# Kernel optimization log

Hardware: AMD Instinct MI355X
Metric: run time of the kernel (lower is better)

## Reference

```python
import jax, jax.numpy as jnp
import numpy as np

LN_EPS = 1e-3  # keras LayerNormalization default epsilon


def setup_inputs() -> dict:
    key = jax.random.key(0)
    ks = jax.random.split(key, 6)
    B, S, D, H, K = 4, 4096, 1024, 16, 64
    scale = 1.0 / np.sqrt(D)
    return {
        "x": jax.random.normal(ks[0], (B, S, D), jnp.float32),
        "Wq": jax.random.normal(ks[1], (D, H, K), jnp.float32) * scale,
        "bq": jnp.zeros((H, K), jnp.float32),
        "Wk": jax.random.normal(ks[2], (D, H, K), jnp.float32) * scale,
        "bk": jnp.zeros((H, K), jnp.float32),
        "Wv": jax.random.normal(ks[3], (D, H, K), jnp.float32) * scale,
        "bv": jnp.zeros((H, K), jnp.float32),
        "Wo": jax.random.normal(ks[4], (H, K, D), jnp.float32) * scale,
        "bo": jnp.zeros((D,), jnp.float32),
        "gamma": jnp.ones((D,), jnp.float32),
        "beta": jnp.zeros((D,), jnp.float32),
        "num_window": 8,
    }


def reference(x, Wq, bq, Wk, bk, Wv, bv, Wo, bo, gamma, beta, num_window):
    B, S, D = x.shape
    H, K = Wq.shape[1], Wq.shape[2]
    Sw = S // num_window
    # Block-diagonal (windowed) attention: reshape seq into windows instead of a Python loop.
    xw = x.reshape(B, num_window, Sw, D)  # [B, W, Sw, D]
    q = jnp.einsum('bwsd,dhk->bwshk', xw, Wq) + bq
    k = jnp.einsum('bwsd,dhk->bwshk', xw, Wk) + bk
    v = jnp.einsum('bwsd,dhk->bwshk', xw, Wv) + bv
    scores = jnp.einsum('bwqhk,bwshk->bwhqs', q, k) / jnp.sqrt(jnp.asarray(K, x.dtype))
    attn = jax.nn.softmax(scores, axis=-1)  # [B, W, H, Sw, Sw]
    ctx = jnp.einsum('bwhqs,bwshk->bwqhk', attn, v)
    attn_out = (jnp.einsum('bwqhk,hkd->bwqd', ctx, Wo) + bo).reshape(B, S, D)
    # residual + layernorm (keras eps=1e-3)
    y = x + attn_out
    mu = jnp.mean(y, axis=-1, keepdims=True)
    var = jnp.mean(jnp.square(y - mu), axis=-1, keepdims=True)
    return (y - mu) * jax.lax.rsqrt(var + LN_EPS) * gamma + beta
```

## Files before the change

### kernel.cpp

```cpp
#include <hip/hip_runtime.h>

typedef __bf16 bf16_t;
typedef __bf16 bf16x4 __attribute__((ext_vector_type(4)));
typedef __bf16 bf16x8 __attribute__((ext_vector_type(8)));
typedef float f32x4 __attribute__((ext_vector_type(4)));

#define MFMA16(a, b, c) __builtin_amdgcn_mfma_f32_16x16x32_bf16((a), (b), (c), 0, 0, 0)

__device__ __forceinline__ void gl_lds16(const bf16_t* g, bf16_t* l) {
  __builtin_amdgcn_global_load_lds(
      (const __attribute__((address_space(1))) void*)g,
      (__attribute__((address_space(3))) void*)l, 16, 0, 0);
}

__global__ __launch_bounds__(256) void cast_x_kernel(const float* __restrict__ x,
                                                     bf16_t* __restrict__ xb) {
  size_t i = (size_t)blockIdx.x * 256 + threadIdx.x;
  float4 v = ((const float4*)x)[i];
  bf16x4 o = {(bf16_t)v.x, (bf16_t)v.y, (bf16_t)v.z, (bf16_t)v.w};
  ((bf16x4*)xb)[i] = o;
}

__global__ __launch_bounds__(256) void transpose_w_kernel(
    const float* __restrict__ Wq, const float* __restrict__ Wk,
    const float* __restrict__ Wv, const float* __restrict__ Wo,
    bf16_t* __restrict__ Wt, bf16_t* __restrict__ WoT) {
  __shared__ bf16_t T[64 * 68];
  const int z = blockIdx.z;
  const float* src = (z == 0) ? Wq : (z == 1) ? Wk : (z == 2) ? Wv : Wo;
  bf16_t* dst = (z < 3) ? (Wt + (size_t)z * 1024 * 1024) : WoT;
  const int tr = blockIdx.y * 64;
  const int tc = blockIdx.x * 64;
  const int tid = threadIdx.x;
#pragma unroll
  for (int it = 0; it < 4; ++it) {
    int t = tid + it * 256;
    int row = t >> 4, c4 = t & 15;
    float4 v = *(const float4*)&src[(size_t)(tr + row) * 1024 + tc + c4 * 4];
    bf16x4 o = {(bf16_t)v.x, (bf16_t)v.y, (bf16_t)v.z, (bf16_t)v.w};
    *(bf16x4*)&T[row * 68 + c4 * 4] = o;
  }
  __syncthreads();
#pragma unroll
  for (int it = 0; it < 2; ++it) {
    int t = tid + it * 256;
    int n = t >> 3, d8 = t & 7;
    bf16x8 o;
#pragma unroll
    for (int j = 0; j < 8; ++j) o[j] = T[(d8 * 8 + j) * 68 + n];
    *(bf16x8*)&dst[(size_t)(tc + n) * 1024 + tr + d8 * 8] = o;
  }
}


__device__ __forceinline__ void stage_half(const bf16_t* __restrict__ g,
                                           bf16_t* l, const int tid) {
#pragma unroll
  for (int j = 0; j < 2; ++j) {
    int idx = j * 512 + tid;
    int row = idx >> 3;
    int c = (idx & 7) ^ (row & 7);
    gl_lds16(g + (size_t)row * 1024 + c * 8, l + idx * 8);
  }
}

__device__ __forceinline__ void gemm256_main(const bf16_t* __restrict__ Ab,
                                             const bf16_t* __restrict__ Bb,
                                             bf16_t* lds, f32x4 (&acc)[8][4],
                                             const int tid) {
  const int l15 = tid & 15, quad = (tid >> 4) & 3;
  const int wv = tid >> 6, wm = wv >> 2, wn = wv & 3;
  const int sx = l15 & 7;
  const int brow0 = (wn & 1) * 64;

  stage_half(Bb, lds + 2 * 8192, tid);
  stage_half(Ab, lds + 0 * 8192, tid);
  stage_half(Bb + 128 * 1024, lds + 3 * 8192, tid);
  stage_half(Ab + 128 * 1024, lds + 1 * 8192, tid);
  stage_half(Bb + 64, lds + 6 * 8192, tid);
  stage_half(Ab + 64, lds + 4 * 8192, tid);
  asm volatile("s_waitcnt vmcnt(4)" ::: "memory");
  __builtin_amdgcn_s_barrier();

  for (int t = 0; t < 16; ++t) {
    bf16_t* const buf = lds + (t & 1) * 32768;
    bf16_t* const nbuf = lds + ((t & 1) ^ 1) * 32768;
    const bf16_t* const Ar = buf + wm * 8192;
    const bf16_t* const Br = buf + (2 + (wn >> 1)) * 8192;

    bf16x8 af[4][2], bfr[4][2];

#pragma unroll
    for (int mf = 0; mf < 4; ++mf)
#pragma unroll
      for (int ks = 0; ks < 2; ++ks)
        af[mf][ks] = *(const bf16x8*)&Ar[(mf * 16 + l15) * 64 +
                                         (((ks * 4 + quad) ^ sx) << 3)];
#pragma unroll
    for (int nf = 0; nf < 2; ++nf)
#pragma unroll
      for (int ks = 0; ks < 2; ++ks)
        bfr[nf][ks] = *(const bf16x8*)&Br[(brow0 + nf * 16 + l15) * 64 +
                                          (((ks * 4 + quad) ^ sx) << 3)];
    if (t + 1 < 16) stage_half(Bb + 128 * 1024 + (t + 1) * 64, nbuf + 3 * 8192, tid);
    __builtin_amdgcn_s_barrier();
    asm volatile("s_waitcnt lgkmcnt(0)" ::: "memory");
    __builtin_amdgcn_s_setprio(1);
#pragma unroll
    for (int mf = 0; mf < 4; ++mf)
#pragma unroll
      for (int nf = 0; nf < 2; ++nf)
#pragma unroll
        for (int ks = 0; ks < 2; ++ks)
          acc[mf][nf] = MFMA16(af[mf][ks], bfr[nf][ks], acc[mf][nf]);
    __builtin_amdgcn_s_setprio(0);
    __builtin_amdgcn_s_barrier();

#pragma unroll
    for (int nf = 2; nf < 4; ++nf)
#pragma unroll
      for (int ks = 0; ks < 2; ++ks)
        bfr[nf][ks] = *(const bf16x8*)&Br[(brow0 + nf * 16 + l15) * 64 +
                                          (((ks * 4 + quad) ^ sx) << 3)];
    if (t + 1 < 16) stage_half(Ab + 128 * 1024 + (t + 1) * 64, nbuf + 1 * 8192, tid);
    __builtin_amdgcn_s_barrier();
    asm volatile("s_waitcnt lgkmcnt(0)" ::: "memory");
    __builtin_amdgcn_s_setprio(1);
#pragma unroll
    for (int mf = 0; mf < 4; ++mf)
#pragma unroll
      for (int nf = 2; nf < 4; ++nf)
#pragma unroll
        for (int ks = 0; ks < 2; ++ks)
          acc[mf][nf] = MFMA16(af[mf][ks], bfr[nf][ks], acc[mf][nf]);
    __builtin_amdgcn_s_setprio(0);
    __builtin_amdgcn_s_barrier();

#pragma unroll
    for (int mf = 0; mf < 4; ++mf)
#pragma unroll
      for (int ks = 0; ks < 2; ++ks)
        af[mf][ks] = *(const bf16x8*)&Ar[((mf + 4) * 16 + l15) * 64 +
                                         (((ks * 4 + quad) ^ sx) << 3)];
    if (t + 2 < 16) stage_half(Bb + (t + 2) * 64, buf + 2 * 8192, tid);
    __builtin_amdgcn_s_barrier();
    asm volatile("s_waitcnt lgkmcnt(0)" ::: "memory");
    __builtin_amdgcn_s_setprio(1);
#pragma unroll
    for (int mf = 0; mf < 4; ++mf)
#pragma unroll
      for (int nf = 2; nf < 4; ++nf)
#pragma unroll
        for (int ks = 0; ks < 2; ++ks)
          acc[mf + 4][nf] = MFMA16(af[mf][ks], bfr[nf][ks], acc[mf + 4][nf]);
    __builtin_amdgcn_s_setprio(0);
    __builtin_amdgcn_s_barrier();

    if (t + 2 < 16) stage_half(Ab + (t + 2) * 64, buf + 0 * 8192, tid);
    __builtin_amdgcn_s_barrier();
    __builtin_amdgcn_s_setprio(1);
#pragma unroll
    for (int mf = 0; mf < 4; ++mf)
#pragma unroll
      for (int nf = 0; nf < 2; ++nf)
#pragma unroll
        for (int ks = 0; ks < 2; ++ks)
          acc[mf + 4][nf] = MFMA16(af[mf][ks], bfr[nf][ks], acc[mf + 4][nf]);
    __builtin_amdgcn_s_setprio(0);
    if (t < 14)
      asm volatile("s_waitcnt vmcnt(4)" ::: "memory");
    else
      asm volatile("s_waitcnt vmcnt(0)" ::: "memory");
    __builtin_amdgcn_s_barrier();
  }
}

__global__ __launch_bounds__(512) void gemm_qkv_kernel(
    const bf16_t* __restrict__ A, const bf16_t* __restrict__ Bt,
    const float* __restrict__ bq, const float* __restrict__ bk,
    const float* __restrict__ bv, bf16_t* __restrict__ C) {
  __shared__ bf16_t lds[2 * 4 * 8192];
  const int tid = threadIdx.x;
  const int lin = blockIdx.x;
  const int swz = (lin & 7) * 96 + (lin >> 3);
  const int bm = swz / 12, bn = swz - bm * 12;

  f32x4 acc[8][4];
#pragma unroll
  for (int i = 0; i < 8; ++i)
#pragma unroll
    for (int j = 0; j < 4; ++j)
#pragma unroll
      for (int e = 0; e < 4; ++e) acc[i][j][e] = 0.f;

  gemm256_main(A + (size_t)(bm * 256) * 1024, Bt + (size_t)(bn * 256) * 1024,
               lds, acc, tid);

  const int l15 = tid & 15, quad = (tid >> 4) & 3;
  const int wv = tid >> 6, wm = wv >> 2, wn = wv & 3;
  const int row0 = bm * 256 + wm * 128 + quad * 4;
  const int col0 = bn * 256 + wn * 64;
#pragma unroll
  for (int nf = 0; nf < 4; ++nf) {
    int col = col0 + nf * 16 + l15;
    float bias, scale;
    if (col < 1024) {
      bias = bq[col];
      scale = 0.125f;
    } else if (col < 2048) {
      bias = bk[col - 1024];
      scale = 1.f;
    } else {
      bias = bv[col - 2048];
      scale = 1.f;
    }
#pragma unroll
    for (int mf = 0; mf < 8; ++mf)
#pragma unroll
      for (int r = 0; r < 4; ++r) {
        int row = row0 + mf * 16 + r;
        C[(size_t)row * 3072 + col] = (bf16_t)((acc[mf][nf][r] + bias) * scale);
      }
  }
}

__global__ __launch_bounds__(256) void attn_kernel(
    const bf16_t* __restrict__ QKV, bf16_t* __restrict__ Ctx) {
  __shared__ bf16_t Ks[64 * 64];
  __shared__ bf16_t Vs[64 * 64];
  __shared__ bf16_t Pb[4][16 * 64];

  const int tid = threadIdx.x;
  const int wv = tid >> 6, quad = (tid >> 4) & 3, l15 = tid & 15;
  const int hid = blockIdx.x, qb = blockIdx.y;
  const int b = hid >> 7, w = (hid >> 4) & 7, h = hid & 15;
  const int rowW = b * 4096 + w * 512;
  const int qbase = qb * 128 + wv * 32;

  bf16x8 qf[2][2];
#pragma unroll
  for (int qt = 0; qt < 2; ++qt) {
    int rowQ = rowW + qbase + qt * 16 + l15;
#pragma unroll
    for (int kh = 0; kh < 2; ++kh)
      qf[qt][kh] = *(const bf16x8*)&QKV[(size_t)rowQ * 3072 + h * 64 + kh * 32 + quad * 8];
  }

  const bf16_t* Kb = QKV + (size_t)rowW * 3072 + 1024 + h * 64;
  const bf16_t* Vg = QKV + (size_t)rowW * 3072 + 2048 + h * 64;

  float lp[2] = {0.f, 0.f};
  f32x4 Oa[2][4];
  f32x4 zero = {0.f, 0.f, 0.f, 0.f};
#pragma unroll
  for (int qt = 0; qt < 2; ++qt)
#pragma unroll
    for (int dt = 0; dt < 4; ++dt) Oa[qt][dt] = zero;

  const int vrow = tid >> 2;
  const int vseg = tid & 3;

  for (int kt = 0; kt < 8; ++kt) {
#pragma unroll
    for (int i = 0; i < 2; ++i) {
      int t = tid + i * 256;
      int row = t >> 3;
      int g = (t & 7) ^ (row & 7);
      gl_lds16(Kb + (size_t)(kt * 64 + row) * 3072 + g * 8, &Ks[t * 8]);
    }
    {
      const bf16_t* src = Vg + (size_t)(kt * 64 + vrow) * 3072 + vseg * 16;
      bf16x8 v0 = *(const bf16x8*)&src[0];
      bf16x8 v1 = *(const bf16x8*)&src[8];
      int sg = vrow >> 3, sr = vrow & 7;
#pragma unroll
      for (int j = 0; j < 8; ++j) {
        int d0 = vseg * 16 + j;
        Vs[d0 * 64 + ((sg ^ (d0 & 7)) << 3) + sr] = v0[j];
        int d1 = vseg * 16 + 8 + j;
        Vs[d1 * 64 + ((sg ^ (d1 & 7)) << 3) + sr] = v1[j];
      }
    }
    __syncthreads();

    bf16x8 kf[4][2], vf[2][4];
#pragma unroll
    for (int jt = 0; jt < 4; ++jt) {
      int key = jt * 16 + l15;
#pragma unroll
      for (int kh = 0; kh < 2; ++kh)
        kf[jt][kh] = *(const bf16x8*)&Ks[key * 64 + (((kh * 4 + quad) ^ (key & 7)) << 3)];
    }
#pragma unroll
    for (int kh = 0; kh < 2; ++kh)
#pragma unroll
      for (int dt = 0; dt < 4; ++dt) {
        int d = dt * 16 + l15;
        vf[kh][dt] = *(const bf16x8*)&Vs[d * 64 + (((kh * 4 + quad) ^ (d & 7)) << 3)];
      }

#pragma unroll
    for (int qt = 0; qt < 2; ++qt) {
      f32x4 st[4];
#pragma unroll
      for (int jt = 0; jt < 4; ++jt) {
        f32x4 a = zero;
#pragma unroll
        for (int kh = 0; kh < 2; ++kh) a = MFMA16(kf[jt][kh], qf[qt][kh], a);
        st[jt] = a;
      }
      float ls = 0.f;
#pragma unroll
      for (int jt = 0; jt < 4; ++jt)
#pragma unroll
        for (int r = 0; r < 4; ++r) {
          float p = __expf(st[jt][r]);
          st[jt][r] = p;
          ls += p;
        }
      lp[qt] += ls;
#pragma unroll
      for (int jt = 0; jt < 4; ++jt) {
        bf16x4 pk = {(bf16_t)st[jt][0], (bf16_t)st[jt][1],
                     (bf16_t)st[jt][2], (bf16_t)st[jt][3]};
        int gs = (jt * 2 + (quad >> 1)) ^ (l15 & 7);
        *(bf16x4*)&Pb[wv][l15 * 64 + gs * 8 + (quad & 1) * 4] = pk;
      }
#pragma unroll
      for (int kh = 0; kh < 2; ++kh) {
        bf16x8 pf = *(const bf16x8*)&Pb[wv][l15 * 64 + (((kh * 4 + quad) ^ (l15 & 7)) << 3)];
#pragma unroll
        for (int dt = 0; dt < 4; ++dt) Oa[qt][dt] = MFMA16(pf, vf[kh][dt], Oa[qt][dt]);
      }
    }
    __syncthreads();
  }

#pragma unroll
  for (int qt = 0; qt < 2; ++qt) {
    float t = lp[qt];
    t += __shfl_xor(t, 16, 64);
    t += __shfl_xor(t, 32, 64);
    float inv_l = 1.0f / t;
    float inv[4];
#pragma unroll
    for (int r = 0; r < 4; ++r) inv[r] = __shfl(inv_l, quad * 4 + r, 64);
#pragma unroll
    for (int dt = 0; dt < 4; ++dt)
#pragma unroll
      for (int r = 0; r < 4; ++r) {
        int orow = rowW + qbase + qt * 16 + quad * 4 + r;
        Ctx[(size_t)orow * 1024 + h * 64 + dt * 16 + l15] = (bf16_t)(Oa[qt][dt][r] * inv[r]);
      }
  }
}

__global__ __launch_bounds__(512) void gemm_proj_kernel(
    const bf16_t* __restrict__ A, const bf16_t* __restrict__ Bt,
    const float* __restrict__ bo, const float* __restrict__ x,
    bf16_t* __restrict__ Yb) {
  __shared__ bf16_t lds[2 * 4 * 8192];
  const int tid = threadIdx.x;
  const int lin = blockIdx.x;
  const int swz = (lin & 7) * 32 + (lin >> 3);
  const int bm = swz >> 2, bn = swz & 3;

  f32x4 acc[8][4];
#pragma unroll
  for (int i = 0; i < 8; ++i)
#pragma unroll
    for (int j = 0; j < 4; ++j)
#pragma unroll
      for (int e = 0; e < 4; ++e) acc[i][j][e] = 0.f;

  gemm256_main(A + (size_t)(bm * 256) * 1024, Bt + (size_t)(bn * 256) * 1024,
               lds, acc, tid);

  const int l15 = tid & 15, quad = (tid >> 4) & 3;
  const int wv = tid >> 6, wm = wv >> 2, wn = wv & 3;
  const int row0 = bm * 256 + wm * 128 + quad * 4;
  const int col0 = bn * 256 + wn * 64;
#pragma unroll
  for (int nf = 0; nf < 4; ++nf) {
    int col = col0 + nf * 16 + l15;
    float bias = bo[col];
#pragma unroll
    for (int mf = 0; mf < 8; ++mf)
#pragma unroll
      for (int r = 0; r < 4; ++r) {
        int row = row0 + mf * 16 + r;
        size_t idx = (size_t)row * 1024 + col;
        Yb[idx] = (bf16_t)(acc[mf][nf][r] + bias + x[idx]);
      }
  }
}

__global__ __launch_bounds__(256) void ln_kernel(const bf16_t* __restrict__ Yb,
                                                 float* __restrict__ Y,
                                                 const float* __restrict__ gamma,
                                                 const float* __restrict__ beta) {
  const int row = blockIdx.x, tid = threadIdx.x;
  bf16x4 yb = ((const bf16x4*)(Yb + (size_t)row * 1024))[tid];
  float y0 = (float)yb[0], y1 = (float)yb[1], y2 = (float)yb[2], y3 = (float)yb[3];
  float s = y0 + y1 + y2 + y3;
  float s2 = y0 * y0 + y1 * y1 + y2 * y2 + y3 * y3;
#pragma unroll
  for (int off = 1; off < 64; off <<= 1) {
    s += __shfl_xor(s, off, 64);
    s2 += __shfl_xor(s2, off, 64);
  }
  __shared__ float red[8];
  int wv = tid >> 6;
  if ((tid & 63) == 0) {
    red[wv] = s;
    red[4 + wv] = s2;
  }
  __syncthreads();
  s = red[0] + red[1] + red[2] + red[3];
  s2 = red[4] + red[5] + red[6] + red[7];
  float mean = s * (1.0f / 1024.0f);
  float var = s2 * (1.0f / 1024.0f) - mean * mean;
  float rs = rsqrtf(var + 1e-3f);
  float4 g = ((const float4*)gamma)[tid];
  float4 bb = ((const float4*)beta)[tid];
  float4 o;
  o.x = (y0 - mean) * rs * g.x + bb.x;
  o.y = (y1 - mean) * rs * g.y + bb.y;
  o.z = (y2 - mean) * rs * g.z + bb.z;
  o.w = (y3 - mean) * rs * g.w + bb.w;
  ((float4*)(Y + (size_t)row * 1024))[tid] = o;
}

extern "C" void kernel_launch(void* const* d_in, const int* in_sizes, int n_in,
                              void* d_out, int out_size, void* d_ws, size_t ws_size,
                              hipStream_t stream) {
  const float* x = (const float*)d_in[0];
  const float* Wq = (const float*)d_in[1];
  const float* bq = (const float*)d_in[2];
  const float* Wk = (const float*)d_in[3];
  const float* bk = (const float*)d_in[4];
  const float* Wv = (const float*)d_in[5];
  const float* bv = (const float*)d_in[6];
  const float* Wo = (const float*)d_in[7];
  const float* bo = (const float*)d_in[8];
  const float* gamma = (const float*)d_in[9];
  const float* beta = (const float*)d_in[10];
  float* Y = (float*)d_out;

  char* ws = (char*)d_ws;
  bf16_t* xb = (bf16_t*)(ws);
  bf16_t* Wt = (bf16_t*)(ws + 33554432);
  bf16_t* WoT = (bf16_t*)(ws + 39845888);
  bf16_t* QKVb = (bf16_t*)(ws + 41943040);
  bf16_t* Ctx = (bf16_t*)(ws + 142606336);
  bf16_t* Yb = (bf16_t*)(ws + 176160768);

  cast_x_kernel<<<16384, 256, 0, stream>>>(x, xb);
  transpose_w_kernel<<<dim3(16, 16, 4), 256, 0, stream>>>(Wq, Wk, Wv, Wo, Wt, WoT);
  gemm_qkv_kernel<<<768, 512, 0, stream>>>(xb, Wt, bq, bk, bv, QKVb);
  attn_kernel<<<dim3(512, 4), 256, 0, stream>>>(QKVb, Ctx);
  gemm_proj_kernel<<<256, 512, 0, stream>>>(Ctx, WoT, bo, x, Yb);
  ln_kernel<<<16384, 256, 0, stream>>>(Yb, Y, gamma, beta);
}
```

Baseline: 420.2 us.

## Split LDS fragment waits in GEMM mainloop and stage epilogues through LDS

Restructures the 256x256 GEMM main loop into an unrolled two-step tile function whose fragment loads are split into halves. This lets MFMAs start after a partial lgkmcnt wait instead of waiting for all LDS reads. Both GEMM epilogues (QKV and output projection) now transpose accumulators through per-wave LDS scratch, so each lane writes contiguous bf16x4 vectors and reads x as float4 instead of scattered 2-byte stores and scalar loads. This adds LDS traffic and extra waits in the epilogue, and reuses the main-loop LDS for scratch. The loop relies on barriers being in place to avoid races.

Measured after the change: 373.1 us. -11.2%, faster.

```diff
diff --git a/kernel.cpp b/kernel.cpp
--- a/kernel.cpp
+++ b/kernel.cpp
@@ -6,6 +6,15 @@
 typedef float f32x4 __attribute__((ext_vector_type(4)));
 
 #define MFMA16(a, b, c) __builtin_amdgcn_mfma_f32_16x16x32_bf16((a), (b), (c), 0, 0, 0)
+
+#define FENCE asm volatile("" ::: "memory")
+#define BAR()                        \
+  do {                               \
+    FENCE;                           \
+    __builtin_amdgcn_s_barrier();    \
+    FENCE;                           \
+  } while (0)
+#define WAITLGKM(n) asm volatile("s_waitcnt lgkmcnt(" #n ")" ::: "memory")
 
 __device__ __forceinline__ void gl_lds16(const bf16_t* g, bf16_t* l) {
   __builtin_amdgcn_global_load_lds(
@@ -64,15 +73,146 @@
   }
 }
 
+__device__ __forceinline__ void tile_step(const int t, bf16_t* const buf,
+                                          bf16_t* const nbuf,
+                                          const bf16_t* __restrict__ Ab,
+                                          const bf16_t* __restrict__ Bb,
+                                          f32x4 (&acc)[8][4], const int tid) {
+  const int l15 = tid & 15, quad = (tid >> 4) & 3;
+  const int wv = tid >> 6, wm = wv >> 2, wn = wv & 3;
+  const int sx = l15 & 7;
+  const int brow0 = (wn & 1) * 64;
+  const bf16_t* const Ar = buf + wm * 8192;
+  const bf16_t* const Br = buf + (2 + (wn >> 1)) * 8192;
+
+  bf16x8 af[4][2], bfr[4][2];
+
+#pragma unroll
+  for (int nf = 0; nf < 2; ++nf)
+#pragma unroll
+    for (int ks = 0; ks < 2; ++ks)
+      bfr[nf][ks] = *(const bf16x8*)&Br[(brow0 + nf * 16 + l15) * 64 +
+                                        (((ks * 4 + quad) ^ sx) << 3)];
+  FENCE;
+#pragma unroll
+  for (int mf = 0; mf < 2; ++mf)
+#pragma unroll
+    for (int ks = 0; ks < 2; ++ks)
+      af[mf][ks] = *(const bf16x8*)&Ar[(mf * 16 + l15) * 64 +
+                                       (((ks * 4 + quad) ^ sx) << 3)];
+  FENCE;
+#pragma unroll
+  for (int mf = 2; mf < 4; ++mf)
+#pragma unroll
+    for (int ks = 0; ks < 2; ++ks)
+      af[mf][ks] = *(const bf16x8*)&Ar[(mf * 16 + l15) * 64 +
+                                       (((ks * 4 + quad) ^ sx) << 3)];
+  FENCE;
+  if (t + 1 < 16) stage_half(Bb + 128 * 1024 + (t + 1) * 64, nbuf + 3 * 8192, tid);
+  BAR();
+  WAITLGKM(4);
+  __builtin_amdgcn_s_setprio(1);
+#pragma unroll
+  for (int ks = 0; ks < 2; ++ks)
+#pragma unroll
+    for (int mf = 0; mf < 2; ++mf)
+#pragma unroll
+      for (int nf = 0; nf < 2; ++nf)
+        acc[mf][nf] = MFMA16(af[mf][ks], bfr[nf][ks], acc[mf][nf]);
+  __builtin_amdgcn_s_setprio(0);
+  WAITLGKM(0);
+  __builtin_amdgcn_s_setprio(1);
+#pragma unroll
+  for (int ks = 0; ks < 2; ++ks)
+#pragma unroll
+    for (int mf = 2; mf < 4; ++mf)
+#pragma unroll
+      for (int nf = 0; nf < 2; ++nf)
+        acc[mf][nf] = MFMA16(af[mf][ks], bfr[nf][ks], acc[mf][nf]);
+  __builtin_amdgcn_s_setprio(0);
+  BAR();
+
+#pragma unroll
+  for (int nf = 2; nf < 4; ++nf)
+#pragma unroll
+    for (int ks = 0; ks < 2; ++ks)
+      bfr[nf][ks] = *(const bf16x8*)&Br[(brow0 + nf * 16 + l15) * 64 +
+                                        (((ks * 4 + quad) ^ sx) << 3)];
+  FENCE;
+  if (t + 1 < 16) stage_half(Ab + 128 * 1024 + (t + 1) * 64, nbuf + 1 * 8192, tid);
+  BAR();
+  WAITLGKM(0);
+  __builtin_amdgcn_s_setprio(1);
+#pragma unroll
+  for (int ks = 0; ks < 2; ++ks)
+#pragma unroll
+    for (int mf = 0; mf < 4; ++mf)
+#pragma unroll
+      for (int nf = 2; nf < 4; ++nf)
+        acc[mf][nf] = MFMA16(af[mf][ks], bfr[nf][ks], acc[mf][nf]);
+  __builtin_amdgcn_s_setprio(0);
+  BAR();
+
+#pragma unroll
+  for (int mf = 0; mf < 2; ++mf)
+#pragma unroll
+    for (int ks = 0; ks < 2; ++ks)
+      af[mf][ks] = *(const bf16x8*)&Ar[((mf + 4) * 16 + l15) * 64 +
+                                       (((ks * 4 + quad) ^ sx) << 3)];
+  FENCE;
+#pragma unroll
+  for (int mf = 2; mf < 4; ++mf)
+#pragma unroll
+    for (int ks = 0; ks < 2; ++ks)
+      af[mf][ks] = *(const bf16x8*)&Ar[((mf + 4) * 16 + l15) * 64 +
+                                       (((ks * 4 + quad) ^ sx) << 3)];
+  FENCE;
+  if (t + 2 < 16) stage_half(Bb + (t + 2) * 64, buf + 2 * 8192, tid);
+  BAR();
+  WAITLGKM(4);
+  __builtin_amdgcn_s_setprio(1);
+#pragma unroll
+  for (int ks = 0; ks < 2; ++ks)
+#pragma unroll
+    for (int mf = 0; mf < 2; ++mf)
+#pragma unroll
+      for (int nf = 2; nf < 4; ++nf)
+        acc[mf + 4][nf] = MFMA16(af[mf][ks], bfr[nf][ks], acc[mf + 4][nf]);
+  __builtin_amdgcn_s_setprio(0);
+  WAITLGKM(0);
+  __builtin_amdgcn_s_setprio(1);
+#pragma unroll
+  for (int ks = 0; ks < 2; ++ks)
+#pragma unroll
+    for (int mf = 2; mf < 4; ++mf)
+#pragma unroll
+      for (int nf = 2; nf < 4; ++nf)
+        acc[mf + 4][nf] = MFMA16(af[mf][ks], bfr[nf][ks], acc[mf + 4][nf]);
+  __builtin_amdgcn_s_setprio(0);
+  BAR();
+
+  if (t + 2 < 16) stage_half(Ab + (t + 2) * 64, buf + 0 * 8192, tid);
+  BAR();
+  __builtin_amdgcn_s_setprio(1);
+#pragma unroll
+  for (int ks = 0; ks < 2; ++ks)
+#pragma unroll
+    for (int mf = 0; mf < 4; ++mf)
+#pragma unroll
+      for (int nf = 0; nf < 2; ++nf)
+        acc[mf + 4][nf] = MFMA16(af[mf][ks], bfr[nf][ks], acc[mf + 4][nf]);
+  __builtin_amdgcn_s_setprio(0);
+  if (t < 14)
+    asm volatile("s_waitcnt vmcnt(4)" ::: "memory");
+  else
+    asm volatile("s_waitcnt vmcnt(0)" ::: "memory");
+  BAR();
+}
+
 __device__ __forceinline__ void gemm256_main(const bf16_t* __restrict__ Ab,
                                              const bf16_t* __restrict__ Bb,
                                              bf16_t* lds, f32x4 (&acc)[8][4],
                                              const int tid) {
-  const int l15 = tid & 15, quad = (tid >> 4) & 3;
-  const int wv = tid >> 6, wm = wv >> 2, wn = wv & 3;
-  const int sx = l15 & 7;
-  const int brow0 = (wn & 1) * 64;
-
   stage_half(Bb, lds + 2 * 8192, tid);
   stage_half(Ab, lds + 0 * 8192, tid);
   stage_half(Bb + 128 * 1024, lds + 3 * 8192, tid);
@@ -80,98 +220,11 @@
   stage_half(Bb + 64, lds + 6 * 8192, tid);
   stage_half(Ab + 64, lds + 4 * 8192, tid);
   asm volatile("s_waitcnt vmcnt(4)" ::: "memory");
-  __builtin_amdgcn_s_barrier();
-
-  for (int t = 0; t < 16; ++t) {
-    bf16_t* const buf = lds + (t & 1) * 32768;
-    bf16_t* const nbuf = lds + ((t & 1) ^ 1) * 32768;
-    const bf16_t* const Ar = buf + wm * 8192;
-    const bf16_t* const Br = buf + (2 + (wn >> 1)) * 8192;
-
-    bf16x8 af[4][2], bfr[4][2];
-
-#pragma unroll
-    for (int mf = 0; mf < 4; ++mf)
-#pragma unroll
-      for (int ks = 0; ks < 2; ++ks)
-        af[mf][ks] = *(const bf16x8*)&Ar[(mf * 16 + l15) * 64 +
-                                         (((ks * 4 + quad) ^ sx) << 3)];
-#pragma unroll
-    for (int nf = 0; nf < 2; ++nf)
-#pragma unroll
-      for (int ks = 0; ks < 2; ++ks)
-        bfr[nf][ks] = *(const bf16x8*)&Br[(brow0 + nf * 16 + l15) * 64 +
-                                          (((ks * 4 + quad) ^ sx) << 3)];
-    if (t + 1 < 16) stage_half(Bb + 128 * 1024 + (t + 1) * 64, nbuf + 3 * 8192, tid);
-    __builtin_amdgcn_s_barrier();
-    asm volatile("s_waitcnt lgkmcnt(0)" ::: "memory");
-    __builtin_amdgcn_s_setprio(1);
-#pragma unroll
-    for (int mf = 0; mf < 4; ++mf)
-#pragma unroll
-      for (int nf = 0; nf < 2; ++nf)
-#pragma unroll
-        for (int ks = 0; ks < 2; ++ks)
-          acc[mf][nf] = MFMA16(af[mf][ks], bfr[nf][ks], acc[mf][nf]);
-    __builtin_amdgcn_s_setprio(0);
-    __builtin_amdgcn_s_barrier();
-
-#pragma unroll
-    for (int nf = 2; nf < 4; ++nf)
-#pragma unroll
-      for (int ks = 0; ks < 2; ++ks)
-        bfr[nf][ks] = *(const bf16x8*)&Br[(brow0 + nf * 16 + l15) * 64 +
-                                          (((ks * 4 + quad) ^ sx) << 3)];
-    if (t + 1 < 16) stage_half(Ab + 128 * 1024 + (t + 1) * 64, nbuf + 1 * 8192, tid);
-    __builtin_amdgcn_s_barrier();
-    asm volatile("s_waitcnt lgkmcnt(0)" ::: "memory");
-    __builtin_amdgcn_s_setprio(1);
-#pragma unroll
-    for (int mf = 0; mf < 4; ++mf)
-#pragma unroll
-      for (int nf = 2; nf < 4; ++nf)
-#pragma unroll
-        for (int ks = 0; ks < 2; ++ks)
-          acc[mf][nf] = MFMA16(af[mf][ks], bfr[nf][ks], acc[mf][nf]);
-    __builtin_amdgcn_s_setprio(0);
-    __builtin_amdgcn_s_barrier();
-
-#pragma unroll
-    for (int mf = 0; mf < 4; ++mf)
-#pragma unroll
-      for (int ks = 0; ks < 2; ++ks)
-        af[mf][ks] = *(const bf16x8*)&Ar[((mf + 4) * 16 + l15) * 64 +
-                                         (((ks * 4 + quad) ^ sx) << 3)];
-    if (t + 2 < 16) stage_half(Bb + (t + 2) * 64, buf + 2 * 8192, tid);
-    __builtin_amdgcn_s_barrier();
-    asm volatile("s_waitcnt lgkmcnt(0)" ::: "memory");
-    __builtin_amdgcn_s_setprio(1);
-#pragma unroll
-    for (int mf = 0; mf < 4; ++mf)
-#pragma unroll
-      for (int nf = 2; nf < 4; ++nf)
-#pragma unroll
-        for (int ks = 0; ks < 2; ++ks)
-          acc[mf + 4][nf] = MFMA16(af[mf][ks], bfr[nf][ks], acc[mf + 4][nf]);
-    __builtin_amdgcn_s_setprio(0);
-    __builtin_amdgcn_s_barrier();
-
-    if (t + 2 < 16) stage_half(Ab + (t + 2) * 64, buf + 0 * 8192, tid);
-    __builtin_amdgcn_s_barrier();
-    __builtin_amdgcn_s_setprio(1);
-#pragma unroll
-    for (int mf = 0; mf < 4; ++mf)
-#pragma unroll
-      for (int nf = 0; nf < 2; ++nf)
-#pragma unroll
-        for (int ks = 0; ks < 2; ++ks)
-          acc[mf + 4][nf] = MFMA16(af[mf][ks], bfr[nf][ks], acc[mf + 4][nf]);
-    __builtin_amdgcn_s_setprio(0);
-    if (t < 14)
-      asm volatile("s_waitcnt vmcnt(4)" ::: "memory");
-    else
-      asm volatile("s_waitcnt vmcnt(0)" ::: "memory");
-    __builtin_amdgcn_s_barrier();
+  BAR();
+
+  for (int t = 0; t < 16; t += 2) {
+    tile_step(t, lds, lds + 32768, Ab, Bb, acc, tid);
+    tile_step(t + 1, lds + 32768, lds, Ab, Bb, acc, tid);
   }
 }
 
@@ -198,29 +251,46 @@
 
   const int l15 = tid & 15, quad = (tid >> 4) & 3;
   const int wv = tid >> 6, wm = wv >> 2, wn = wv & 3;
-  const int row0 = bm * 256 + wm * 128 + quad * 4;
   const int col0 = bn * 256 + wn * 64;
+  const int rbase = bm * 256 + wm * 128;
+  float* R = (float*)(lds + wv * 8192);
+
+  float wbias[4], wscale[4];
 #pragma unroll
   for (int nf = 0; nf < 4; ++nf) {
     int col = col0 + nf * 16 + l15;
-    float bias, scale;
     if (col < 1024) {
-      bias = bq[col];
-      scale = 0.125f;
+      wbias[nf] = bq[col];
+      wscale[nf] = 0.125f;
     } else if (col < 2048) {
-      bias = bk[col - 1024];
-      scale = 1.f;
+      wbias[nf] = bk[col - 1024];
+      wscale[nf] = 1.f;
     } else {
-      bias = bv[col - 2048];
-      scale = 1.f;
-    }
-#pragma unroll
-    for (int mf = 0; mf < 8; ++mf)
-#pragma unroll
-      for (int r = 0; r < 4; ++r) {
-        int row = row0 + mf * 16 + r;
-        C[(size_t)row * 3072 + col] = (bf16_t)((acc[mf][nf][r] + bias) * scale);
-      }
+      wbias[nf] = bv[col - 2048];
+      wscale[nf] = 1.f;
+    }
+  }
+#pragma unroll
+  for (int p = 0; p < 4; ++p) {
+#pragma unroll
+    for (int mfi = 0; mfi < 2; ++mfi) {
+#pragma unroll
+      for (int nf = 0; nf < 4; ++nf)
+#pragma unroll
+        for (int r = 0; r < 4; ++r)
+          R[(mfi * 16 + quad * 4 + r) * 68 + nf * 16 + l15] =
+              (acc[p * 2 + mfi][nf][r] + wbias[nf]) * wscale[nf];
+    }
+    WAITLGKM(0);
+#pragma unroll
+    for (int i = 0; i < 8; ++i) {
+      const int lr = i * 4 + quad;
+      f32x4 vv = *(const f32x4*)&R[lr * 68 + l15 * 4];
+      bf16x4 o = {(bf16_t)vv[0], (bf16_t)vv[1], (bf16_t)vv[2], (bf16_t)vv[3]};
+      int row = rbase + p * 32 + lr;
+      *(bf16x4*)&C[(size_t)row * 3072 + col0 + l15 * 4] = o;
+    }
+    WAITLGKM(0);
   }
 }
 
@@ -378,20 +448,34 @@
 
   const int l15 = tid & 15, quad = (tid >> 4) & 3;
   const int wv = tid >> 6, wm = wv >> 2, wn = wv & 3;
-  const int row0 = bm * 256 + wm * 128 + quad * 4;
   const int col0 = bn * 256 + wn * 64;
-#pragma unroll
-  for (int nf = 0; nf < 4; ++nf) {
-    int col = col0 + nf * 16 + l15;
-    float bias = bo[col];
-#pragma unroll
-    for (int mf = 0; mf < 8; ++mf)
-#pragma unroll
-      for (int r = 0; r < 4; ++r) {
-        int row = row0 + mf * 16 + r;
-        size_t idx = (size_t)row * 1024 + col;
-        Yb[idx] = (bf16_t)(acc[mf][nf][r] + bias + x[idx]);
-      }
+  const int rbase = bm * 256 + wm * 128;
+  float* R = (float*)(lds + wv * 8192);
+  const int colg = col0 + l15 * 4;
+  const float4 bo4 = *(const float4*)&bo[colg];
+
+#pragma unroll
+  for (int p = 0; p < 4; ++p) {
+#pragma unroll
+    for (int mfi = 0; mfi < 2; ++mfi) {
+#pragma unroll
+      for (int nf = 0; nf < 4; ++nf)
+#pragma unroll
+        for (int r = 0; r < 4; ++r)
+          R[(mfi * 16 + quad * 4 + r) * 68 + nf * 16 + l15] = acc[p * 2 + mfi][nf][r];
+    }
+    WAITLGKM(0);
+#pragma unroll
+    for (int i = 0; i < 8; ++i) {
+      const int lr = i * 4 + quad;
+      int row = rbase + p * 32 + lr;
+      f32x4 vv = *(const f32x4*)&R[lr * 68 + l15 * 4];
+      float4 xv = *(const float4*)&x[(size_t)row * 1024 + colg];
+      bf16x4 o = {(bf16_t)(vv[0] + bo4.x + xv.x), (bf16_t)(vv[1] + bo4.y + xv.y),
+                  (bf16_t)(vv[2] + bo4.z + xv.z), (bf16_t)(vv[3] + bo4.w + xv.w)};
+      *(bf16x4*)&Yb[(size_t)row * 1024 + colg] = o;
+    }
+    WAITLGKM(0);
   }
 }
 
```
